# Kernel optimization log

Measured on AMD Instinct MI355X. Metric: run time of the kernel, lower is better.

## Reference

```python
import jax, jax.numpy as jnp
import numpy as np

B, T, I, H, V = 32, 64, 512, 512, 32000


def setup_inputs() -> dict:
    key = jax.random.key(0)
    ks = jax.random.split(key, 8)
    s_in = 1.0 / np.sqrt(H)  # torch LSTMCell/Linear uniform init scale
    return {
        "isequence": jax.random.normal(ks[0], (B, T, I), dtype=jnp.float32),
        "hidden_t": jax.random.normal(ks[1], (B, H), dtype=jnp.float32),
        "W_ih": jax.random.uniform(ks[2], (4 * H, I), jnp.float32, -s_in, s_in),
        "W_hh": jax.random.uniform(ks[3], (4 * H, H), jnp.float32, -s_in, s_in),
        "b_ih": jax.random.uniform(ks[4], (4 * H,), jnp.float32, -s_in, s_in),
        "b_hh": jax.random.uniform(ks[5], (4 * H,), jnp.float32, -s_in, s_in),
        "W_out": jax.random.uniform(ks[6], (V, H), jnp.float32, -s_in, s_in),
        "b_out": jax.random.uniform(ks[7], (V,), jnp.float32, -s_in, s_in),
    }


def reference(isequence, hidden_t, W_ih, W_hh, b_ih, b_hh, W_out, b_out):
    # isequence: [B, T, I] -> time-major [T, B, I] (matches permute(1,0,2))
    xs = jnp.transpose(isequence, (1, 0, 2))
    # Precompute input-to-gate projections for all timesteps: [T, B, 4H]
    x_gates = jnp.einsum("tbi,gi->tbg", xs, W_ih) + b_ih + b_hh
    c0 = jnp.zeros_like(hidden_t)  # init_hidden zeros cell state

    def step(carry, xg):
        h, c = carry
        gates = xg + h @ W_hh.T  # [B, 4H], torch gate order: i, f, g, o
        i_g, f_g, g_g, o_g = jnp.split(gates, 4, axis=-1)
        i_g = jax.nn.sigmoid(i_g)
        f_g = jax.nn.sigmoid(f_g)
        g_g = jnp.tanh(g_g)
        o_g = jax.nn.sigmoid(o_g)
        c_new = f_g * c + i_g * g_g
        h_new = o_g * jnp.tanh(c_new)
        logits = h_new @ W_out.T + b_out  # [B, V]
        return (h_new, c_new), logits

    _, osequence = jax.lax.scan(step, (hidden_t, c0), x_gates)  # [T, B, V]
    return jnp.transpose(osequence, (1, 0, 2))  # [B, T, V]
```

## Files before the change

### kernel.cpp

```cpp
#include <hip/hip_runtime.h>
#include <hip/hip_bf16.h>

typedef unsigned short u16;
typedef unsigned int u32;
typedef __attribute__((ext_vector_type(4))) float f32x4;
typedef __attribute__((ext_vector_type(8))) short short8;
typedef __attribute__((ext_vector_type(4))) unsigned short u16x4;
typedef __attribute__((ext_vector_type(4))) unsigned int u32x4;

#define LSTM_NBLK 16
#define LSTM_GRID 240

static __device__ __forceinline__ u16 f2bf(float f) {
  union { float f; unsigned u; } v; v.f = f;
  unsigned r = v.u + 0x7FFFu + ((v.u >> 16) & 1u);
  return (u16)(r >> 16);
}

static __device__ __forceinline__ void gload_lds16(const void* g, void* l) {
  __builtin_amdgcn_global_load_lds(
      (const __attribute__((address_space(1))) unsigned int*)g,
      (__attribute__((address_space(3))) unsigned int*)l, 16, 0, 0);
}

static __device__ __forceinline__ short8 ld_b128_sc(const void* p) {
  short8 r;
  asm volatile("global_load_dwordx4 %0, %1, off sc0 sc1"
               : "=v"(r) : "v"(p) : "memory");
  return r;
}
static __device__ __forceinline__ unsigned ld_u32_sc_wait(const unsigned* p) {
  unsigned r;
  asm volatile("global_load_dword %0, %1, off sc0 sc1\n\ts_waitcnt vmcnt(0)"
               : "=v"(r) : "v"(p) : "memory");
  return r;
}
static __device__ __forceinline__ void st_u32_sc(void* p, unsigned v) {
  asm volatile("global_store_dword %0, %1, off sc0 sc1"
               :: "v"(p), "v"(v) : "memory");
}
static __device__ __forceinline__ void waitcnt0() {
  asm volatile("s_waitcnt vmcnt(0)" ::: "memory");
  __builtin_amdgcn_sched_barrier(0);
}

__global__ void prep_kernel(const float* __restrict__ iseq, const float* __restrict__ h0,
                            const float* __restrict__ wih, const float* __restrict__ whh,
                            u16* __restrict__ wih_bf, u16* __restrict__ whh_bf,
                            u16* __restrict__ ax, u32* __restrict__ h2u,
                            unsigned* __restrict__ flags) {
  const int S0 = 262144;
  const int S1 = S0 + 262144;
  const int S2 = S1 + 262144;
  const int S3 = S2 + 8192;
  const int S4 = S3 + 4096;
  int u = blockIdx.x * blockDim.x + threadIdx.x;
  int stride = gridDim.x * blockDim.x;
  for (; u < S4; u += stride) {
    if (u < S0) {
      int e = u * 4; f32x4 v = *(const f32x4*)(wih + e);
      u16x4 o; o[0]=f2bf(v[0]); o[1]=f2bf(v[1]); o[2]=f2bf(v[2]); o[3]=f2bf(v[3]);
      *(u16x4*)(wih_bf + e) = o;
    } else if (u < S1) {
      int e = (u - S0) * 4; f32x4 v = *(const f32x4*)(whh + e);
      u16x4 o; o[0]=f2bf(v[0]); o[1]=f2bf(v[1]); o[2]=f2bf(v[2]); o[3]=f2bf(v[3]);
      *(u16x4*)(whh_bf + e) = o;
    } else if (u < S2) {
      int e = (u - S1) * 4; int m = e >> 9; int k = e & 511;
      int b = m & 31; int t = m >> 5;
      f32x4 v = *(const f32x4*)(iseq + ((b * 64 + t) << 9) + k);
      u16x4 o; o[0]=f2bf(v[0]); o[1]=f2bf(v[1]); o[2]=f2bf(v[2]); o[3]=f2bf(v[3]);
      *(u16x4*)(ax + e) = o;
    } else if (u < S3) {
      int v = u - S2;
      int e = v * 2;
      float lo = h0[e], hi = h0[e + 1];
      h2u[v] = (((u32)f2bf(hi)) << 16) | (u32)f2bf(lo);
    } else {
      flags[u - S3] = 0u;
    }
  }
}

__global__ __launch_bounds__(256, 2) void gemm_bt(
    const u16* __restrict__ A, const u16* __restrict__ Bw,
    float* __restrict__ C, const float* __restrict__ bias1,
    const float* __restrict__ bias2, int N, int remap) {
  __shared__ u16 As[2][8192];
  __shared__ u16 Bs[2][8192];
  const int tid = threadIdx.x;
  const int w = tid >> 6, l = tid & 63;
  const int wr = w >> 1, wc = w & 1;
  const int lid = blockIdx.x;
  const int cpx = gridDim.x >> 3;
  const int lid2 = (lid & 7) * cpx + (lid >> 3);
  const int tn = (lid2 >> 4) * 128;
  const int tm = (lid2 & 15) * 128;

  f32x4 acc[4][4];
#pragma unroll
  for (int i = 0; i < 4; ++i)
#pragma unroll
    for (int j = 0; j < 4; ++j) acc[i][j] = (f32x4){0.f, 0.f, 0.f, 0.f};

  auto stage = [&](int buf, int kt) {
#pragma unroll
    for (int i = 0; i < 4; ++i) {
      int r = (w * 4 + i) * 8 + (l >> 3);
      int c16 = (l & 7) ^ (r & 7);
      int rowm = tm + r;
      const u16* srca;
      if (remap) {
        srca = A + ((rowm & 63) + 1) * 16384 + (rowm >> 6) * 512 + kt * 64 + c16 * 8;
      } else {
        srca = A + rowm * 512 + kt * 64 + c16 * 8;
      }
      gload_lds16(srca, &As[buf][(w * 4 + i) * 512]);
      const u16* srcb = Bw + (tn + r) * 512 + kt * 64 + c16 * 8;
      gload_lds16(srcb, &Bs[buf][(w * 4 + i) * 512]);
    }
  };

  stage(0, 0);
  int buf = 0;
  for (int kt = 0; kt < 8; ++kt) {
    __syncthreads();
    if (kt < 7) stage(buf ^ 1, kt + 1);
#pragma unroll
    for (int kk = 0; kk < 2; ++kk) {
      short8 af[4], bfr[4];
#pragma unroll
      for (int mi = 0; mi < 4; ++mi) {
        int row = wr * 64 + mi * 16 + (l & 15);
        int s = (kk * 4 + (l >> 4)) ^ (row & 7);
        af[mi] = *(const short8*)&As[buf][row * 64 + s * 8];
      }
#pragma unroll
      for (int ni = 0; ni < 4; ++ni) {
        int row = wc * 64 + ni * 16 + (l & 15);
        int s = (kk * 4 + (l >> 4)) ^ (row & 7);
        bfr[ni] = *(const short8*)&Bs[buf][row * 64 + s * 8];
      }
#pragma unroll
      for (int mi = 0; mi < 4; ++mi)
#pragma unroll
        for (int ni = 0; ni < 4; ++ni)
          acc[mi][ni] = __builtin_amdgcn_mfma_f32_16x16x32_bf16(
              af[mi], bfr[ni], acc[mi][ni], 0, 0, 0);
    }
    buf ^= 1;
  }

#pragma unroll
  for (int ni = 0; ni < 4; ++ni) {
    int gcol = tn + wc * 64 + ni * 16 + (l & 15);
    float bv = 0.f;
    if (bias1) bv += bias1[gcol];
    if (bias2) bv += bias2[gcol];
#pragma unroll
    for (int mi = 0; mi < 4; ++mi) {
      int grow0 = tm + wr * 64 + mi * 16 + ((l >> 4) << 2);
      f32x4 a = acc[mi][ni];
#pragma unroll
      for (int q = 0; q < 4; ++q) {
        C[(long long)(grow0 + q) * N + gcol] = a[q] + bv;
      }
    }
  }
}

__global__ __launch_bounds__(512, 1) void lstm_persist(
    const u16* __restrict__ whh, const float* __restrict__ xg,
    u16* __restrict__ h2, unsigned* __restrict__ flags,
    const float* __restrict__ wout, u16* __restrict__ wout_bf) {
  __shared__ u16 hbuf[32 * 512];
  __shared__ u16 hloc[1024];
  const int tid = threadIdx.x;

  if (blockIdx.x >= LSTM_NBLK) {
    int idx = (blockIdx.x - LSTM_NBLK) * 512 + tid;
    int stride = (LSTM_GRID - LSTM_NBLK) * 512;
    for (int u2 = idx; u2 < 4096000; u2 += stride) {
      int e = u2 * 4; f32x4 v = *(const f32x4*)(wout + e);
      u16x4 o; o[0]=f2bf(v[0]); o[1]=f2bf(v[1]); o[2]=f2bf(v[2]); o[3]=f2bf(v[3]);
      *(u16x4*)(wout_bf + e) = o;
    }
    return;
  }

  const int w = tid >> 6, l = tid & 63;
  const int blk = blockIdx.x;
  const int j0 = (blk * 8 + w) * 4;
  const int c = l & 15;
  const int wrow = (c >> 2) * 512 + j0 + (c & 3);
  const int ko = (l >> 4) * 8;
  u32* h2u = (u32*)h2;

  short8 bfr[16];
  const u16* wp = whh + wrow * 512 + ko;
#pragma unroll
  for (int kt = 0; kt < 16; ++kt) bfr[kt] = *(const short8*)(wp + kt * 32);

  const int rq = (l >> 4) * 4;
  const int jj = l & 3;
  const int b0 = l & 15, b1 = 16 + (l & 15);
  const int s0 = b0 & 7;

  const int cb = tid & 31;
  const int ckg = tid >> 5;
  const int csw = cb & 7;

  const int ob = tid >> 4;
  const int oj = tid & 15;

  float creg[2][4];
#pragma unroll
  for (int mt = 0; mt < 2; ++mt)
#pragma unroll
    for (int q = 0; q < 4; ++q) creg[mt][q] = 0.f;

  float xcur[2][4], xnext[2][4];
#pragma unroll
  for (int mt = 0; mt < 2; ++mt)
#pragma unroll
    for (int q = 0; q < 4; ++q)
      xcur[mt][q] = xg[(mt * 16 + rq + q) * 2048 + wrow];

  for (int it = 0; it < 64; ++it) {
    if (it > 0 && w == 0) {
      const unsigned want = (unsigned)it;
      for (;;) {
        unsigned f = ld_u32_sc_wait(flags + blk * 256 + (l & 15) * 16);
        if (__all((int)(f >= want))) break;
      }
    }
    __syncthreads();

    {
      const u16* src = h2 + it * 16384 + cb * 512 + ckg * 32;
      short8 d0 = ld_b128_sc(src);
      short8 d1 = ld_b128_sc(src + 8);
      short8 d2 = ld_b128_sc(src + 16);
      short8 d3 = ld_b128_sc(src + 24);
      waitcnt0();
      *(short8*)&hbuf[cb * 512 + (((ckg * 4 + 0) ^ csw) * 8)] = d0;
      *(short8*)&hbuf[cb * 512 + (((ckg * 4 + 1) ^ csw) * 8)] = d1;
      *(short8*)&hbuf[cb * 512 + (((ckg * 4 + 2) ^ csw) * 8)] = d2;
      *(short8*)&hbuf[cb * 512 + (((ckg * 4 + 3) ^ csw) * 8)] = d3;
    }
    __syncthreads();

    f32x4 acc0 = (f32x4){0.f, 0.f, 0.f, 0.f};
    f32x4 acc1 = (f32x4){0.f, 0.f, 0.f, 0.f};
#pragma unroll
    for (int kt = 0; kt < 16; ++kt) {
      int x = ((kt * 4 + (l >> 4)) ^ s0) * 8;
      short8 a0 = *(const short8*)&hbuf[b0 * 512 + x];
      short8 a1 = *(const short8*)&hbuf[b1 * 512 + x];
      acc0 = __builtin_amdgcn_mfma_f32_16x16x32_bf16(a0, bfr[kt], acc0, 0, 0, 0);
      acc1 = __builtin_amdgcn_mfma_f32_16x16x32_bf16(a1, bfr[kt], acc1, 0, 0, 0);
    }
    if (it < 63) {
#pragma unroll
      for (int mt = 0; mt < 2; ++mt)
#pragma unroll
        for (int q = 0; q < 4; ++q)
          xnext[mt][q] = xg[((it + 1) * 32 + mt * 16 + rq + q) * 2048 + wrow];
    }

#pragma unroll
    for (int mt = 0; mt < 2; ++mt) {
#pragma unroll
      for (int q = 0; q < 4; ++q) {
        float av = (mt == 0) ? acc0[q] : acc1[q];
        float gp = av + xcur[mt][q];
        int bl = (l & 48) | jj;
        float xi = __shfl(gp, bl);
        float xf = __shfl(gp, bl | 4);
        float xgg = __shfl(gp, bl | 8);
        float xo = __shfl(gp, bl | 12);
        float is = 1.f / (1.f + __expf(-xi));
        float fs = 1.f / (1.f + __expf(-xf));
        float e2 = __expf(2.f * xgg);
        float gt = 1.f - 2.f / (e2 + 1.f);
        float os = 1.f / (1.f + __expf(-xo));
        float cn = fs * creg[mt][q] + is * gt;
        creg[mt][q] = cn;
        float e2c = __expf(2.f * cn);
        float hn = os * (1.f - 2.f / (e2c + 1.f));
        if ((l & 12) == 0) {
          int b = mt * 16 + rq + q;
          hloc[b * 32 + w * 4 + jj] = f2bf(hn);
        }
      }
    }
    __syncthreads();

    {
      u32 v = *(const u32*)&hloc[ob * 32 + oj * 2];
      st_u32_sc(h2u + (it + 1) * 8192 + ob * 256 + blk * 16 + oj, v);
      waitcnt0();
    }
    __syncthreads();

    if (it < 63) {
      if (w == 0 && l < 16)
        st_u32_sc(flags + l * 256 + blk * 16, (unsigned)(it + 1));
#pragma unroll
      for (int mt = 0; mt < 2; ++mt)
#pragma unroll
        for (int q = 0; q < 4; ++q)
          xcur[mt][q] = xnext[mt][q];
    }
  }
}

extern "C" void kernel_launch(void* const* d_in, const int* in_sizes, int n_in,
                              void* d_out, int out_size, void* d_ws, size_t ws_size,
                              hipStream_t stream) {
  (void)in_sizes; (void)n_in; (void)out_size; (void)ws_size;
  const float* iseq = (const float*)d_in[0];
  const float* h0   = (const float*)d_in[1];
  const float* wih  = (const float*)d_in[2];
  const float* whh  = (const float*)d_in[3];
  const float* bih  = (const float*)d_in[4];
  const float* bhh  = (const float*)d_in[5];
  const float* wout = (const float*)d_in[6];
  const float* bout = (const float*)d_in[7];

  char* ws = (char*)d_ws;
  u16* wout_bf = (u16*)(ws + 0);
  u16* wih_bf  = (u16*)(ws + 32768000);
  u16* whh_bf  = (u16*)(ws + 34865152);
  u16* ax      = (u16*)(ws + 36962304);
  u16* h2      = (u16*)(ws + 39059456);
  unsigned* flags = (unsigned*)(ws + 41189376);
  float* xg    = (float*)(ws + 41254912);
  float* out   = (float*)d_out;

  prep_kernel<<<2048, 256, 0, stream>>>(iseq, h0, wih, whh,
                                        wih_bf, whh_bf, ax, (u32*)h2, flags);
  gemm_bt<<<256, 256, 0, stream>>>(ax, wih_bf, xg, bih, bhh, 2048, 0);
  lstm_persist<<<LSTM_GRID, 512, 0, stream>>>(whh_bf, xg, h2, flags,
                                              wout, wout_bf);
  gemm_bt<<<4000, 256, 0, stream>>>(h2, wout_bf, out, bout, nullptr, 32000, 1);
}
```

Baseline: 546.0 us.

## Add 256x128-tile triple-buffered output-projection GEMM kernel

Adds a dedicated kernel for the large vocabulary projection. It uses 512 threads, a 256x128 output tile and a three-slot LDS pipeline with explicit vmcnt waits, replacing the 128x128 double-buffered generic GEMM, which loses its remap path. The larger M tile halves how often the W_out tiles are re-read, and the deeper prefetch hides more load latency. In exchange it uses more LDS and allows one block per CU, which lowers occupancy.

Result: no change. 540.1 us (-1.1%).

```diff
diff --git a/kernel.cpp b/kernel.cpp
--- a/kernel.cpp
+++ b/kernel.cpp
@@ -85,7 +85,7 @@
 __global__ __launch_bounds__(256, 2) void gemm_bt(
     const u16* __restrict__ A, const u16* __restrict__ Bw,
     float* __restrict__ C, const float* __restrict__ bias1,
-    const float* __restrict__ bias2, int N, int remap) {
+    const float* __restrict__ bias2, int N) {
   __shared__ u16 As[2][8192];
   __shared__ u16 Bs[2][8192];
   const int tid = threadIdx.x;
@@ -108,13 +108,7 @@
     for (int i = 0; i < 4; ++i) {
       int r = (w * 4 + i) * 8 + (l >> 3);
       int c16 = (l & 7) ^ (r & 7);
-      int rowm = tm + r;
-      const u16* srca;
-      if (remap) {
-        srca = A + ((rowm & 63) + 1) * 16384 + (rowm >> 6) * 512 + kt * 64 + c16 * 8;
-      } else {
-        srca = A + rowm * 512 + kt * 64 + c16 * 8;
-      }
+      const u16* srca = A + (tm + r) * 512 + kt * 64 + c16 * 8;
       gload_lds16(srca, &As[buf][(w * 4 + i) * 512]);
       const u16* srcb = Bw + (tn + r) * 512 + kt * 64 + c16 * 8;
       gload_lds16(srcb, &Bs[buf][(w * 4 + i) * 512]);
@@ -157,6 +151,98 @@
     float bv = 0.f;
     if (bias1) bv += bias1[gcol];
     if (bias2) bv += bias2[gcol];
+#pragma unroll
+    for (int mi = 0; mi < 4; ++mi) {
+      int grow0 = tm + wr * 64 + mi * 16 + ((l >> 4) << 2);
+      f32x4 a = acc[mi][ni];
+#pragma unroll
+      for (int q = 0; q < 4; ++q) {
+        C[(long long)(grow0 + q) * N + gcol] = a[q] + bv;
+      }
+    }
+  }
+}
+
+__global__ __launch_bounds__(512, 1) void gemm2_256(
+    const u16* __restrict__ A, const u16* __restrict__ Bw,
+    float* __restrict__ C, const float* __restrict__ bias, int N) {
+  __shared__ u16 Asl[3][16384];
+  __shared__ u16 Bsl[3][8192];
+  const int tid = threadIdx.x;
+  const int w = tid >> 6, l = tid & 63;
+  const int wr = w >> 1, wc = w & 1;
+  const int lid = blockIdx.x;
+  const int cpx = gridDim.x >> 3;
+  const int lid2 = (lid & 7) * cpx + (lid >> 3);
+  const int tm = (lid2 & 7) * 256;
+  const int tn = (lid2 >> 3) * 128;
+
+  f32x4 acc[4][4];
+#pragma unroll
+  for (int i = 0; i < 4; ++i)
+#pragma unroll
+    for (int j = 0; j < 4; ++j) acc[i][j] = (f32x4){0.f, 0.f, 0.f, 0.f};
+
+  auto stage = [&](int slot, int kt) {
+#pragma unroll
+    for (int j = 0; j < 4; ++j) {
+      int chunk = w * 4 + j;
+      int r = chunk * 8 + (l >> 3);
+      int c16 = (l & 7) ^ (r & 7);
+      int rowm = tm + r;
+      const u16* srca = A + ((rowm & 63) + 1) * 16384 + (rowm >> 6) * 512
+                          + kt * 64 + c16 * 8;
+      gload_lds16(srca, &Asl[slot][chunk * 512]);
+    }
+#pragma unroll
+    for (int j = 0; j < 2; ++j) {
+      int chunk = w * 2 + j;
+      int r = chunk * 8 + (l >> 3);
+      int c16 = (l & 7) ^ (r & 7);
+      const u16* srcb = Bw + (tn + r) * 512 + kt * 64 + c16 * 8;
+      gload_lds16(srcb, &Bsl[slot][chunk * 512]);
+    }
+  };
+
+  stage(0, 0);
+  stage(1, 1);
+  for (int kt = 0; kt < 8; ++kt) {
+    const int slot = kt % 3;
+    if (kt < 7) {
+      asm volatile("s_waitcnt vmcnt(6)" ::: "memory");
+    } else {
+      asm volatile("s_waitcnt vmcnt(0)" ::: "memory");
+    }
+    __builtin_amdgcn_sched_barrier(0);
+    __builtin_amdgcn_s_barrier();
+    __builtin_amdgcn_sched_barrier(0);
+    if (kt < 6) stage((kt + 2) % 3, kt + 2);
+#pragma unroll
+    for (int kk = 0; kk < 2; ++kk) {
+      short8 bfr[4];
+#pragma unroll
+      for (int ni = 0; ni < 4; ++ni) {
+        int row = wc * 64 + ni * 16 + (l & 15);
+        int s = (kk * 4 + (l >> 4)) ^ (row & 7);
+        bfr[ni] = *(const short8*)&Bsl[slot][row * 64 + s * 8];
+      }
+#pragma unroll
+      for (int mi = 0; mi < 4; ++mi) {
+        int row = wr * 64 + mi * 16 + (l & 15);
+        int s = (kk * 4 + (l >> 4)) ^ (row & 7);
+        short8 af = *(const short8*)&Asl[slot][row * 64 + s * 8];
+#pragma unroll
+        for (int ni = 0; ni < 4; ++ni)
+          acc[mi][ni] = __builtin_amdgcn_mfma_f32_16x16x32_bf16(
+              af, bfr[ni], acc[mi][ni], 0, 0, 0);
+      }
+    }
+  }
+
+#pragma unroll
+  for (int ni = 0; ni < 4; ++ni) {
+    int gcol = tn + wc * 64 + ni * 16 + (l & 15);
+    float bv = bias[gcol];
 #pragma unroll
     for (int mi = 0; mi < 4; ++mi) {
       int grow0 = tm + wr * 64 + mi * 16 + ((l >> 4) << 2);
@@ -340,8 +426,8 @@
 
   prep_kernel<<<2048, 256, 0, stream>>>(iseq, h0, wih, whh,
                                         wih_bf, whh_bf, ax, (u32*)h2, flags);
-  gemm_bt<<<256, 256, 0, stream>>>(ax, wih_bf, xg, bih, bhh, 2048, 0);
+  gemm_bt<<<256, 256, 0, stream>>>(ax, wih_bf, xg, bih, bhh, 2048);
   lstm_persist<<<LSTM_GRID, 512, 0, stream>>>(whh_bf, xg, h2, flags,
                                               wout, wout_bf);
-  gemm_bt<<<4000, 256, 0, stream>>>(h2, wout_bf, out, bout, nullptr, 32000, 1);
-}
+  gemm2_256<<<2000, 512, 0, stream>>>(h2, wout_bf, out, bout, 32000);
+}
```
